# Kernel tuning notes

Hardware: AMD Instinct MI355X
Metric: run time of the kernel (lower is better)

The kernel has to match this reference:

```python
import jax, jax.numpy as jnp
import numpy as np

B, T, H = 4096, 8, 512


def setup_inputs() -> dict:
    key = jax.random.key(0)
    ks = jax.random.split(key, 14)
    s = 1.0 / np.sqrt(H)
    u = lambda k, shape: jax.random.uniform(k, shape, jnp.float32, -s, s)
    return {
        "inps": jax.random.normal(ks[0], (B, T, H), jnp.float32),
        "enc_output": jax.random.normal(ks[1], (B, T, H), jnp.float32),
        "conv_w": u(ks[2], (1, T, 1)),   # Conv1d(tuple_len,1,1) weight
        "conv_b": u(ks[3], (1,)),
        "Wih": u(ks[4], (4 * H, H)),      # LSTM input weights (i,f,g,o)
        "Whh": u(ks[5], (4 * H, H)),
        "bih": u(ks[6], (4 * H,)),
        "bhh": u(ks[7], (4 * H,)),
        "W1": u(ks[8], (H, H)),           # attn.W1
        "b1": u(ks[9], (H,)),
        "W2": u(ks[10], (H, H)),          # attn.W2
        "b2": u(ks[11], (H,)),
        "vw": u(ks[12], (1, H)),          # attn.v
        "vb": u(ks[13], (1,)),
    }


def reference(inps, enc_output, conv_w, conv_b, Wih, Whh, bih, bhh, W1, b1, W2, b2, vw, vb):
    Bv, Tv, Hv = enc_output.shape
    # Conv1d(tuple_len -> 1, kernel 1): mix over the tuple (channel) dim
    inp0 = jnp.einsum('bch,c->bh', enc_output, conv_w[0, :, 0]) + conv_b[0]  # [B,H]
    # W1 @ E is step-invariant: hoist out of the decode loop (same math)
    W1E = jnp.einsum('bth,oh->bto', enc_output, W1) + b1  # [B,T,H]
    bidx = jnp.arange(Bv)

    def step(carry, _):
        h, c, mask, inp = carry
        # single-layer LSTM cell, torch gate order i,f,g,o
        gates = inp @ Wih.T + bih + h @ Whh.T + bhh  # [B,4H]
        i_, f_, g_, o_ = jnp.split(gates, 4, axis=-1)
        c = jax.nn.sigmoid(f_) * c + jax.nn.sigmoid(i_) * jnp.tanh(g_)
        h = jax.nn.sigmoid(o_) * jnp.tanh(c)  # di
        # additive attention: v(tanh(W1 E + W2 di))
        Ui = jnp.einsum('bth,h->bt', jnp.tanh(W1E + (h @ W2.T + b2)[:, None, :]), vw[0]) + vb[0]
        ai = jax.nn.softmax(Ui, axis=1)
        ai = jnp.where(mask, -jnp.inf, ai)  # masking happens AFTER softmax, as in source
        ptr = jnp.argmax(ai, axis=1)  # [B]
        mask = mask.at[bidx, ptr].set(True)
        inp = inps[bidx, ptr]  # gather next decoder input
        return (h, c, mask, inp), (Ui, ptr)

    h0 = jnp.zeros((Bv, Hv), inps.dtype)
    c0 = jnp.zeros_like(h0)
    mask0 = jnp.zeros((Bv, Tv), dtype=bool)
    # first torch step uses mask=None, equivalent to an all-False mask -> uniform scan
    _, (Uis, ptrs) = jax.lax.scan(step, (h0, c0, mask0, inp0), None, length=Tv)
    probs = jnp.transpose(Uis, (1, 0, 2))  # [B, T, T]
    ptrs = jnp.transpose(ptrs, (1, 0))     # [B, T]
    return probs, ptrs
```

## Files before the change

### kernel.cpp

```cpp
#include <hip/hip_runtime.h>
#include <hip/hip_bf16.h>

#define Bn 4096
#define Tn 8
#define Hn 512

typedef __attribute__((ext_vector_type(8))) _Float16 half8v;
typedef __attribute__((ext_vector_type(4))) float f32x4;

__device__ __forceinline__ float sigm(float x) { return 0.5f * tanhf(0.5f * x) + 0.5f; }

__device__ __forceinline__ short f2h(float x) {
    _Float16 h = (_Float16)x;
    return *reinterpret_cast<short*>(&h);
}
__device__ __forceinline__ float h2f(short s) {
    _Float16 h = *reinterpret_cast<_Float16*>(&s);
    return (float)h;
}
__device__ __forceinline__ void split2(float x, short& hi, short& lo) {
    hi = f2h(x);
    lo = f2h((x - h2f(hi)) * 4096.0f);
}

#define GLOAD16(g, l) __builtin_amdgcn_global_load_lds( \
    (const __attribute__((address_space(1))) unsigned int*)(g), \
    (__attribute__((address_space(3))) unsigned int*)(l), 16, 0, 0)


__global__ __launch_bounds__(256) void k_prep(const float* __restrict__ Wih,
                                              const float* __restrict__ Whh,
                                              const float* __restrict__ bih,
                                              const float* __restrict__ bhh,
                                              short* __restrict__ WcatHi,
                                              short* __restrict__ WcatLo,
                                              float* __restrict__ bcat) {
    int tid = blockIdx.x * 256 + threadIdx.x;
    int jp = tid >> 10, k = tid & 1023;
    int g = (jp >> 4) & 3;
    int h = (jp & 15) + ((jp >> 6) << 4);
    int j = g * 512 + h;
    float v = (k < 512) ? Wih[j * 512 + k] : Whh[j * 512 + (k - 512)];
    short hi, lo; split2(v, hi, lo);
    WcatHi[tid] = hi; WcatLo[tid] = lo;
    if (k == 0) bcat[jp] = bih[j] + bhh[j];
}

__global__ __launch_bounds__(256) void k_split4(const float* __restrict__ x,
                                                short* __restrict__ hi,
                                                short* __restrict__ lo, int n4) {
    int i = blockIdx.x * 256 + threadIdx.x;
    if (i >= n4) return;
    float4 v = ((const float4*)x)[i];
    short h0, l0, h1, l1, h2, l2, h3, l3;
    split2(v.x, h0, l0); split2(v.y, h1, l1);
    split2(v.z, h2, l2); split2(v.w, h3, l3);
    ((short4*)hi)[i] = make_short4(h0, h1, h2, h3);
    ((short4*)lo)[i] = make_short4(l0, l1, l2, l3);
}

__global__ __launch_bounds__(256) void k_init(const float* __restrict__ enc,
                                              const float* __restrict__ cw,
                                              const float* __restrict__ cb,
                                              short* __restrict__ Xhi,
                                              short* __restrict__ Xlo,
                                              float* __restrict__ C,
                                              int* __restrict__ mask) {
    int tid = blockIdx.x * 256 + threadIdx.x;
    int b = tid >> 9, h = tid & 511;
    float s = cb[0];
    const float* e = enc + ((size_t)b << 12) + h;
#pragma unroll
    for (int t = 0; t < Tn; ++t) s = fmaf(e[t * Hn], cw[t], s);
    short hi, lo; split2(s, hi, lo);
    size_t xb = ((size_t)b << 10) + h;
    Xhi[xb] = hi; Xlo[xb] = lo;
    Xhi[xb + 512] = 0; Xlo[xb + 512] = 0;
    C[tid] = 0.0f;
    if (h == 0) mask[b] = 0;
}

template <int NW, bool FUSE, int SWZ>
__global__ __launch_bounds__(256) void gemm_t(
    const short* __restrict__ Ahi, const short* __restrict__ Alo, int lda,
    const short* __restrict__ Whi, const short* __restrict__ Wlo,
    const float* __restrict__ bias, float* __restrict__ out,
    float* __restrict__ Cst, short* __restrict__ Xh, short* __restrict__ Xl,
    int N, int K) {
    constexpr int BN = 32 * NW;
    constexpr int BUFSH = (256 + 2 * BN) * 32;
    __shared__ short sm[2 * BUFSH];

    int bx = blockIdx.x, by = blockIdx.y;
    if constexpr (SWZ == 1) {
        int w = bx + (by << 4), c = w & 7, k = w >> 3;
        by = ((c >> 1) << 3) | (k >> 3);
        bx = ((c & 1) << 3) | (k & 7);
    } else if constexpr (SWZ == 2) {
        int w = bx + (by << 2), c = w & 7, k = w >> 3;
        by = (c << 5) | (k >> 2);
        bx = k & 3;
    } else if constexpr (SWZ == 3) {
        int w = bx + (by << 3), c = w & 7, k = w >> 3;
        by = ((c >> 1) << 3) | (k >> 2);
        bx = ((c & 1) << 2) | (k & 3);
    }

    const int tid = threadIdx.x;
    const int lane = tid & 63;
    const int wv = tid >> 6;
    const int wm = wv >> 1, wn = wv & 1;
    const int lm = lane & 15, lk = lane >> 4;
    const int m0 = by * 128, n0 = bx * BN;

    const int sq = lane & 3;
    const int srow = wv * 16 + (lane >> 2);

    f32x4 acc[4][NW] = {};
    f32x4 acc2[4][NW] = {};

    float bb[NW];
#pragma unroll
    for (int j = 0; j < NW; ++j) bb[j] = bias[n0 + wn * (16 * NW) + j * 16 + lm];

    auto STAGE = [&](int buf, int k0) {
        short* base = sm + buf * BUFSH;
#pragma unroll
        for (int half = 0; half < 2; ++half) {
            int r = half * 64 + srow;
            int qg = sq ^ ((r >> 1) & 3);
            size_t aoff = (size_t)(m0 + r) * lda + k0 + qg * 8;
            int lb = half * 2048 + wv * 512;
            GLOAD16(Ahi + aoff, base + lb);
            GLOAD16(Alo + aoff, base + 128 * 32 + lb);
        }
#pragma unroll
        for (int half = 0; half < BN / 64; ++half) {
            int r = half * 64 + srow;
            int qg = sq ^ ((r >> 1) & 3);
            size_t boff = (size_t)(n0 + r) * K + k0 + qg * 8;
            int lb = half * 2048 + wv * 512;
            GLOAD16(Whi + boff, base + 256 * 32 + lb);
            GLOAD16(Wlo + boff, base + (256 + BN) * 32 + lb);
        }
    };

    STAGE(0, 0);
    int cur = 0;
    for (int k0 = 0; k0 < K; k0 += 32) {
        __syncthreads();
        if (k0 + 32 < K) STAGE(cur ^ 1, k0 + 32);

        short* smAhi = sm + cur * BUFSH;
        short* smAlo = smAhi + 128 * 32;
        short* smBhi = smAhi + 256 * 32;
        short* smBlo = smAhi + (256 + BN) * 32;

        half8v ahi[4], alo[4], bhi[NW], blo[NW];
#pragma unroll
        for (int i = 0; i < 4; ++i) {
            int ra = wm * 64 + i * 16 + lm;
            int offa = ra * 32 + (lk ^ ((ra >> 1) & 3)) * 8;
            ahi[i] = *(const half8v*)&smAhi[offa];
            alo[i] = *(const half8v*)&smAlo[offa];
        }
#pragma unroll
        for (int j = 0; j < NW; ++j) {
            int rb = wn * (16 * NW) + j * 16 + lm;
            int offb = rb * 32 + (lk ^ ((rb >> 1) & 3)) * 8;
            bhi[j] = *(const half8v*)&smBhi[offb];
            blo[j] = *(const half8v*)&smBlo[offb];
        }
#pragma unroll
        for (int i = 0; i < 4; ++i)
#pragma unroll
            for (int j = 0; j < NW; ++j) {
                acc[i][j]  = __builtin_amdgcn_mfma_f32_16x16x32_f16(ahi[i], bhi[j], acc[i][j], 0, 0, 0);
                acc2[i][j] = __builtin_amdgcn_mfma_f32_16x16x32_f16(ahi[i], blo[j], acc2[i][j], 0, 0, 0);
                acc2[i][j] = __builtin_amdgcn_mfma_f32_16x16x32_f16(alo[i], bhi[j], acc2[i][j], 0, 0, 0);
            }
        cur ^= 1;
    }

    const float ls = 1.0f / 4096.0f;

    if constexpr (FUSE) {
        const int h = lm + 16 * ((n0 >> 6) + wn);
#pragma unroll
        for (int i = 0; i < 4; ++i) {
#pragma unroll
            for (int r = 0; r < 4; ++r) {
                int brow = m0 + wm * 64 + i * 16 + lk * 4 + r;
                float gi = acc[i][0][r] + ls * acc2[i][0][r] + bb[0];
                float gf = acc[i][1][r] + ls * acc2[i][1][r] + bb[1];
                float gg = acc[i][2][r] + ls * acc2[i][2][r] + bb[2];
                float go = acc[i][3][r] + ls * acc2[i][3][r] + bb[3];
                size_t ch = ((size_t)brow << 9) + h;
                float c = sigm(gf) * Cst[ch] + sigm(gi) * tanhf(gg);
                float hn = sigm(go) * tanhf(c);
                Cst[ch] = c;
                short shi, slo; split2(hn, shi, slo);
                size_t xb = ((size_t)brow << 10) + 512 + h;
                Xh[xb] = shi; Xl[xb] = slo;
            }
        }
    } else {
        __syncthreads();
        constexpr int SW = 16 * NW + 4;
        float* tile = reinterpret_cast<float*>(sm) + wv * 16 * SW;
        constexpr int LPR = 4 * NW;
        const int rl = lane / LPR, cc = lane % LPR;
#pragma unroll
        for (int i = 0; i < 4; ++i) {
#pragma unroll
            for (int j = 0; j < NW; ++j)
#pragma unroll
                for (int r = 0; r < 4; ++r)
                    tile[(lk * 4 + r) * SW + j * 16 + lm] = acc[i][j][r] + ls * acc2[i][j][r] + bb[j];
            constexpr int RPS = 64 / LPR;
#pragma unroll
            for (int s = 0; s < 16 / RPS; ++s) {
                int row = s * RPS + rl;
                float4 v = *(float4*)&tile[row * SW + cc * 4];
                *(float4*)(out + (size_t)(m0 + wm * 64 + i * 16 + row) * N +
                           n0 + wn * (16 * NW) + cc * 4) = v;
            }
        }
    }
}

__global__ __launch_bounds__(256) void k_attn(const float* __restrict__ W1E,
                                              const float* __restrict__ W2h,
                                              const float* __restrict__ vw,
                                              const float* __restrict__ vbp,
                                              const float* __restrict__ inps,
                                              short* __restrict__ Xhi,
                                              short* __restrict__ Xlo,
                                              int* __restrict__ mask,
                                              float* __restrict__ probs,
                                              float* __restrict__ ptrs,
                                              int step) {
    const int b = blockIdx.x;
    const int tid = threadIdx.x;
    const int lane = tid & 63;
    const int wv = tid >> 6;
    __shared__ float sU[Tn];
    __shared__ int sptr;

    const float4* w2p = (const float4*)(W2h + (size_t)b * Hn + lane * 8);
    float4 w2a = w2p[0], w2b = w2p[1];
    const float4* vp = (const float4*)(vw + lane * 8);
    float4 va = vp[0], vb4 = vp[1];
    float vbias = vbp[0];

#pragma unroll
    for (int q = 0; q < 2; ++q) {
        int t = wv * 2 + q;
        const float4* w1 = (const float4*)(W1E + ((size_t)b << 12) + t * Hn + lane * 8);
        float4 u0 = w1[0], u1 = w1[1];
        float p = va.x * tanhf(u0.x + w2a.x) + va.y * tanhf(u0.y + w2a.y)
                + va.z * tanhf(u0.z + w2a.z) + va.w * tanhf(u0.w + w2a.w)
                + vb4.x * tanhf(u1.x + w2b.x) + vb4.y * tanhf(u1.y + w2b.y)
                + vb4.z * tanhf(u1.z + w2b.z) + vb4.w * tanhf(u1.w + w2b.w);
#pragma unroll
        for (int off = 32; off; off >>= 1) p += __shfl_down(p, off, 64);
        if (lane == 0) sU[t] = p + vbias;
    }
    __syncthreads();

    if (tid == 0) {
        int mk = mask[b];
        float best = -1e30f;
        int ptr = 0;
#pragma unroll
        for (int t = 0; t < Tn; ++t) {
            probs[(size_t)b * 64 + step * 8 + t] = sU[t];
            if (!((mk >> t) & 1) && sU[t] > best) { best = sU[t]; ptr = t; }
        }
        mask[b] = mk | (1 << ptr);
        ptrs[(size_t)b * 8 + step] = (float)ptr;
        sptr = ptr;
    }
    __syncthreads();
    const float2* src = (const float2*)(inps + ((size_t)b << 12) + (size_t)sptr * Hn);
    float2 v = src[tid];
    short h0, l0, h1, l1;
    split2(v.x, h0, l0); split2(v.y, h1, l1);
    size_t xb = ((size_t)b << 10) + tid * 2;
    *(short2*)&Xhi[xb] = make_short2(h0, h1);
    *(short2*)&Xlo[xb] = make_short2(l0, l1);
}

extern "C" void kernel_launch(void* const* d_in, const int* in_sizes, int n_in,
                              void* d_out, int out_size, void* d_ws, size_t ws_size,
                              hipStream_t stream) {
    const float* inps  = (const float*)d_in[0];
    const float* enc   = (const float*)d_in[1];
    const float* convw = (const float*)d_in[2];
    const float* convb = (const float*)d_in[3];
    const float* Wih   = (const float*)d_in[4];
    const float* Whh   = (const float*)d_in[5];
    const float* bih   = (const float*)d_in[6];
    const float* bhh   = (const float*)d_in[7];
    const float* W1    = (const float*)d_in[8];
    const float* b1    = (const float*)d_in[9];
    const float* W2    = (const float*)d_in[10];
    const float* b2    = (const float*)d_in[11];
    const float* vw    = (const float*)d_in[12];
    const float* vb    = (const float*)d_in[13];

    float* out   = (float*)d_out;
    float* probs = out;
    float* ptrs  = out + (size_t)Bn * 64;

    char* wsb = (char*)d_ws;
    float* W1E    = (float*)wsb;
    short* encHi  = (short*)(wsb + (64ull << 20));
    short* encLo  = (short*)(wsb + (96ull << 20));
    short* Xhi1   = (short*)(wsb + (64ull << 20));
    short* Xlo1   = (short*)(wsb + (72ull << 20));
    float* W2h    = (float*)(wsb + (96ull << 20));
    float* C      = (float*)(wsb + (104ull << 20));
    short* Xhi0   = (short*)(wsb + (112ull << 20));
    short* Xlo0   = (short*)(wsb + (120ull << 20));
    short* WcatHi = (short*)(wsb + (128ull << 20));
    short* WcatLo = (short*)(wsb + (132ull << 20));
    short* W1hi   = (short*)(wsb + (136ull << 20));
    short* W1lo   = (short*)(wsb + (136ull << 20) + (512u << 10));
    short* W2hi   = (short*)(wsb + (137ull << 20));
    short* W2lo   = (short*)(wsb + (137ull << 20) + (512u << 10));
    float* bcat   = (float*)(wsb + (138ull << 20));
    int*   mask   = (int*)(wsb + (138ull << 20) + (16u << 10));

    k_prep<<<(2048 * 1024) / 256, 256, 0, stream>>>(Wih, Whh, bih, bhh, WcatHi, WcatLo, bcat);
    k_split4<<<(Bn * Tn * Hn / 4) / 256, 256, 0, stream>>>(enc, encHi, encLo, Bn * Tn * Hn / 4);
    k_split4<<<(Hn * Hn / 4) / 256, 256, 0, stream>>>(W1, W1hi, W1lo, Hn * Hn / 4);
    k_split4<<<(Hn * Hn / 4) / 256, 256, 0, stream>>>(W2, W2hi, W2lo, Hn * Hn / 4);

    gemm_t<4, false, 2><<<dim3(Hn / 128, (Bn * Tn) / 128), 256, 0, stream>>>(
        encHi, encLo, Hn, W1hi, W1lo, b1, W1E, nullptr, nullptr, nullptr, Hn, Hn);

    k_init<<<(Bn * Hn) / 256, 256, 0, stream>>>(enc, convw, convb, Xhi0, Xlo0, C, mask);

    for (int step = 0; step < Tn; ++step) {
        short* Xh_cur = (step & 1) ? Xhi1 : Xhi0;
        short* Xl_cur = (step & 1) ? Xlo1 : Xlo0;
        short* Xh_nxt = (step & 1) ? Xhi0 : Xhi1;
        short* Xl_nxt = (step & 1) ? Xlo0 : Xlo1;

        gemm_t<4, true, 1><<<dim3(2048 / 128, Bn / 128), 256, 0, stream>>>(
            Xh_cur, Xl_cur, 1024, WcatHi, WcatLo, bcat, nullptr, C, Xh_nxt, Xl_nxt, 2048, 1024);
        gemm_t<2, false, 3><<<dim3(Hn / 64, Bn / 128), 256, 0, stream>>>(
            Xh_nxt + 512, Xl_nxt + 512, 1024, W2hi, W2lo, b2, W2h, nullptr, nullptr, nullptr, Hn, Hn);
        k_attn<<<Bn, 256, 0, stream>>>(W1E, W2h, vw, vb, inps, Xh_nxt, Xl_nxt, mask, probs, ptrs, step);
    }
}
```

Measured before the change: 940.8 us.

## Double GEMM block to 512 threads with 32-row warp tiles

The split-fp16 MFMA GEMM now runs with 8 waves per block instead of 4. Each wave owns a 32-row by BN/2 tile instead of 64 rows, which halves the per-wave accumulator registers. Staging is simplified to one 16-byte load per thread per operand. The goal is more resident waves to hide LDS and global latency, at the cost of less register-level reuse of B fragments and more LDS reads per MFMA.

```diff
diff --git a/kernel.cpp b/kernel.cpp
--- a/kernel.cpp
+++ b/kernel.cpp
@@ -81,14 +81,15 @@
 }
 
 template <int NW, bool FUSE, int SWZ>
-__global__ __launch_bounds__(256) void gemm_t(
+__global__ __launch_bounds__(512) void gemm_t(
     const short* __restrict__ Ahi, const short* __restrict__ Alo, int lda,
     const short* __restrict__ Whi, const short* __restrict__ Wlo,
     const float* __restrict__ bias, float* __restrict__ out,
     float* __restrict__ Cst, short* __restrict__ Xh, short* __restrict__ Xl,
     int N, int K) {
     constexpr int BN = 32 * NW;
-    constexpr int BUFSH = (256 + 2 * BN) * 32;
+    constexpr int NJ = NW;
+    constexpr int BUFSH = 8192 + 2 * BN * 32;
     __shared__ short sm[2 * BUFSH];
 
     int bx = blockIdx.x, by = blockIdx.y;
@@ -109,39 +110,33 @@
     const int tid = threadIdx.x;
     const int lane = tid & 63;
     const int wv = tid >> 6;
-    const int wm = wv >> 1, wn = wv & 1;
+    const int wm = wv >> 1;
+    const int wn = wv & 1;
     const int lm = lane & 15, lk = lane >> 4;
     const int m0 = by * 128, n0 = bx * BN;
 
-    const int sq = lane & 3;
-    const int srow = wv * 16 + (lane >> 2);
-
-    f32x4 acc[4][NW] = {};
-    f32x4 acc2[4][NW] = {};
-
-    float bb[NW];
-#pragma unroll
-    for (int j = 0; j < NW; ++j) bb[j] = bias[n0 + wn * (16 * NW) + j * 16 + lm];
+    f32x4 acc[2][NJ] = {};
+    f32x4 acc2[2][NJ] = {};
+
+    float bb[NJ];
+#pragma unroll
+    for (int j = 0; j < NJ; ++j) bb[j] = bias[n0 + wn * (BN >> 1) + j * 16 + lm];
 
     auto STAGE = [&](int buf, int k0) {
         short* base = sm + buf * BUFSH;
-#pragma unroll
-        for (int half = 0; half < 2; ++half) {
-            int r = half * 64 + srow;
-            int qg = sq ^ ((r >> 1) & 3);
-            size_t aoff = (size_t)(m0 + r) * lda + k0 + qg * 8;
-            int lb = half * 2048 + wv * 512;
-            GLOAD16(Ahi + aoff, base + lb);
-            GLOAD16(Alo + aoff, base + 128 * 32 + lb);
-        }
-#pragma unroll
-        for (int half = 0; half < BN / 64; ++half) {
-            int r = half * 64 + srow;
-            int qg = sq ^ ((r >> 1) & 3);
-            size_t boff = (size_t)(n0 + r) * K + k0 + qg * 8;
-            int lb = half * 2048 + wv * 512;
-            GLOAD16(Whi + boff, base + 256 * 32 + lb);
-            GLOAD16(Wlo + boff, base + (256 + BN) * 32 + lb);
+        {
+            int row = tid >> 2, sq = tid & 3;
+            int qg = sq ^ ((row >> 1) & 3);
+            size_t aoff = (size_t)(m0 + row) * lda + k0 + qg * 8;
+            GLOAD16(Ahi + aoff, base + tid * 8);
+            GLOAD16(Alo + aoff, base + 4096 + tid * 8);
+        }
+        if (BN == 128 || tid < BN * 4) {
+            int row = tid >> 2, sq = tid & 3;
+            int qg = sq ^ ((row >> 1) & 3);
+            size_t boff = (size_t)(n0 + row) * K + k0 + qg * 8;
+            GLOAD16(Whi + boff, base + 8192 + tid * 8);
+            GLOAD16(Wlo + boff, base + 8192 + BN * 32 + tid * 8);
         }
     };
 
@@ -151,30 +146,26 @@
         __syncthreads();
         if (k0 + 32 < K) STAGE(cur ^ 1, k0 + 32);
 
-        short* smAhi = sm + cur * BUFSH;
-        short* smAlo = smAhi + 128 * 32;
-        short* smBhi = smAhi + 256 * 32;
-        short* smBlo = smAhi + (256 + BN) * 32;
-
-        half8v ahi[4], alo[4], bhi[NW], blo[NW];
-#pragma unroll
-        for (int i = 0; i < 4; ++i) {
-            int ra = wm * 64 + i * 16 + lm;
+        short* base = sm + cur * BUFSH;
+        half8v ahi[2], alo[2], bhi[NJ], blo[NJ];
+#pragma unroll
+        for (int i = 0; i < 2; ++i) {
+            int ra = wm * 32 + i * 16 + lm;
             int offa = ra * 32 + (lk ^ ((ra >> 1) & 3)) * 8;
-            ahi[i] = *(const half8v*)&smAhi[offa];
-            alo[i] = *(const half8v*)&smAlo[offa];
-        }
-#pragma unroll
-        for (int j = 0; j < NW; ++j) {
-            int rb = wn * (16 * NW) + j * 16 + lm;
+            ahi[i] = *(const half8v*)&base[offa];
+            alo[i] = *(const half8v*)&base[4096 + offa];
+        }
+#pragma unroll
+        for (int j = 0; j < NJ; ++j) {
+            int rb = wn * (BN >> 1) + j * 16 + lm;
             int offb = rb * 32 + (lk ^ ((rb >> 1) & 3)) * 8;
-            bhi[j] = *(const half8v*)&smBhi[offb];
-            blo[j] = *(const half8v*)&smBlo[offb];
-        }
-#pragma unroll
-        for (int i = 0; i < 4; ++i)
-#pragma unroll
-            for (int j = 0; j < NW; ++j) {
+            bhi[j] = *(const half8v*)&base[8192 + offb];
+            blo[j] = *(const half8v*)&base[8192 + BN * 32 + offb];
+        }
+#pragma unroll
+        for (int i = 0; i < 2; ++i)
+#pragma unroll
+            for (int j = 0; j < NJ; ++j) {
                 acc[i][j]  = __builtin_amdgcn_mfma_f32_16x16x32_f16(ahi[i], bhi[j], acc[i][j], 0, 0, 0);
                 acc2[i][j] = __builtin_amdgcn_mfma_f32_16x16x32_f16(ahi[i], blo[j], acc2[i][j], 0, 0, 0);
                 acc2[i][j] = __builtin_amdgcn_mfma_f32_16x16x32_f16(alo[i], bhi[j], acc2[i][j], 0, 0, 0);
@@ -187,10 +178,10 @@
     if constexpr (FUSE) {
         const int h = lm + 16 * ((n0 >> 6) + wn);
 #pragma unroll
-        for (int i = 0; i < 4; ++i) {
+        for (int i = 0; i < 2; ++i) {
 #pragma unroll
             for (int r = 0; r < 4; ++r) {
-                int brow = m0 + wm * 64 + i * 16 + lk * 4 + r;
+                int brow = m0 + wm * 32 + i * 16 + lk * 4 + r;
                 float gi = acc[i][0][r] + ls * acc2[i][0][r] + bb[0];
                 float gf = acc[i][1][r] + ls * acc2[i][1][r] + bb[1];
                 float gg = acc[i][2][r] + ls * acc2[i][2][r] + bb[2];
@@ -206,14 +197,14 @@
         }
     } else {
         __syncthreads();
-        constexpr int SW = 16 * NW + 4;
+        constexpr int SW = 16 * NJ + 4;
         float* tile = reinterpret_cast<float*>(sm) + wv * 16 * SW;
-        constexpr int LPR = 4 * NW;
+        constexpr int LPR = 4 * NJ;
         const int rl = lane / LPR, cc = lane % LPR;
 #pragma unroll
-        for (int i = 0; i < 4; ++i) {
-#pragma unroll
-            for (int j = 0; j < NW; ++j)
+        for (int i = 0; i < 2; ++i) {
+#pragma unroll
+            for (int j = 0; j < NJ; ++j)
 #pragma unroll
                 for (int r = 0; r < 4; ++r)
                     tile[(lk * 4 + r) * SW + j * 16 + lm] = acc[i][j][r] + ls * acc2[i][j][r] + bb[j];
@@ -222,8 +213,8 @@
             for (int s = 0; s < 16 / RPS; ++s) {
                 int row = s * RPS + rl;
                 float4 v = *(float4*)&tile[row * SW + cc * 4];
-                *(float4*)(out + (size_t)(m0 + wm * 64 + i * 16 + row) * N +
-                           n0 + wn * (16 * NW) + cc * 4) = v;
+                *(float4*)(out + (size_t)(m0 + wm * 32 + i * 16 + row) * N +
+                           n0 + wn * (BN >> 1) + cc * 4) = v;
             }
         }
     }
@@ -337,7 +328,7 @@
     k_split4<<<(Hn * Hn / 4) / 256, 256, 0, stream>>>(W1, W1hi, W1lo, Hn * Hn / 4);
     k_split4<<<(Hn * Hn / 4) / 256, 256, 0, stream>>>(W2, W2hi, W2lo, Hn * Hn / 4);
 
-    gemm_t<4, false, 2><<<dim3(Hn / 128, (Bn * Tn) / 128), 256, 0, stream>>>(
+    gemm_t<4, false, 2><<<dim3(Hn / 128, (Bn * Tn) / 128), 512, 0, stream>>>(
         encHi, encLo, Hn, W1hi, W1lo, b1, W1E, nullptr, nullptr, nullptr, Hn, Hn);
 
     k_init<<<(Bn * Hn) / 256, 256, 0, stream>>>(enc, convw, convb, Xhi0, Xlo0, C, mask);
@@ -348,9 +339,9 @@
         short* Xh_nxt = (step & 1) ? Xhi0 : Xhi1;
         short* Xl_nxt = (step & 1) ? Xlo0 : Xlo1;
 
-        gemm_t<4, true, 1><<<dim3(2048 / 128, Bn / 128), 256, 0, stream>>>(
+        gemm_t<4, true, 1><<<dim3(2048 / 128, Bn / 128), 512, 0, stream>>>(
             Xh_cur, Xl_cur, 1024, WcatHi, WcatLo, bcat, nullptr, C, Xh_nxt, Xl_nxt, 2048, 1024);
-        gemm_t<2, false, 3><<<dim3(Hn / 64, Bn / 128), 256, 0, stream>>>(
+        gemm_t<2, false, 3><<<dim3(Hn / 64, Bn / 128), 512, 0, stream>>>(
             Xh_nxt + 512, Xl_nxt + 512, 1024, W2hi, W2lo, b2, W2h, nullptr, nullptr, nullptr, Hn, Hn);
         k_attn<<<Bn, 256, 0, stream>>>(W1E, W2h, vw, vb, inps, Xh_nxt, Xl_nxt, mask, probs, ptrs, step);
     }
```

New measurement: 879.4 us. 6.5% less time.
